# Kernel tuning notes

Measured on AMD Instinct MI355X. Metric: run time of the kernel, lower is better.

The kernel has to match this reference:

```python
import jax, jax.numpy as jnp
import numpy as np

DIM = 1024
NUM_HEADS = 16
HEAD_DIM = DIM // NUM_HEADS  # 64; only used for the softmax scale


def setup_inputs() -> dict:
    key = jax.random.key(0)
    ks = jax.random.split(key, 9)
    s = 1.0 / np.sqrt(DIM)
    return {
        "x": jax.random.normal(ks[0], (2, 4096, DIM), dtype=jnp.float32),
        "Wq": jax.random.normal(ks[1], (DIM, DIM), dtype=jnp.float32) * s,
        "bq": jnp.zeros((DIM,), dtype=jnp.float32),
        "Wk": jax.random.normal(ks[2], (DIM, DIM), dtype=jnp.float32) * s,
        "bk": jnp.zeros((DIM,), dtype=jnp.float32),
        "Wv": jax.random.normal(ks[3], (DIM, DIM), dtype=jnp.float32) * s,
        "bv": jnp.zeros((DIM,), dtype=jnp.float32),
        "Wo": jax.random.normal(ks[4], (DIM, DIM), dtype=jnp.float32) * s,
        "bo": jnp.zeros((DIM,), dtype=jnp.float32),
    }


def reference(x, Wq, bq, Wk, bk, Wv, bv, Wo, bo):
    # Projections (nn.Linear equivalents)
    q = jnp.einsum("bsd,df->bsf", x, Wq) + bq
    k = jnp.einsum("bsd,df->bsf", x, Wk) + bk
    v = jnp.einsum("bsd,df->bsf", x, Wv) + bv
    # Full-dim attention (no head split); scale uses head_dim per original code.
    scale = 1.0 / np.sqrt(HEAD_DIM)
    scores = jnp.einsum("bqd,bkd->bqk", q, k) * scale  # [B, S, S]
    attn = jax.nn.softmax(scores, axis=-1)
    out = jnp.einsum("bqk,bkd->bqd", attn, v)
    return jnp.einsum("bsd,df->bsf", out, Wo) + bo
```

## Files before the change

kernel.cpp:

```cpp
#include <hip/hip_runtime.h>

typedef unsigned short u16;
using bf16x8  = __attribute__((ext_vector_type(8))) __bf16;
using floatx4 = __attribute__((ext_vector_type(4))) float;

__device__ __forceinline__ u16 f2bf(float f) {
  unsigned int u = __builtin_bit_cast(unsigned int, f);
  u += 0x7fffu + ((u >> 16) & 1u);
  return (u16)(u >> 16);
}
__device__ __forceinline__ float bf2f(u16 h) {
  unsigned int u = ((unsigned int)h) << 16;
  return __builtin_bit_cast(float, u);
}

#define AS1(p) ((const __attribute__((address_space(1))) void*)(p))
#define AS3(p) ((__attribute__((address_space(3))) void*)(p))

#define NE2_PROLOGUE(bmv, bnv)                                               \
  __shared__ u16 lds[36864];                          \
  const int tid = threadIdx.x;                                               \
  const int w = tid >> 6, lane = tid & 63;                                   \
  const int wm = (w >> 2) * 64, wn = (w & 3) * 64;                           \
  const int wm4 = (w >> 2) * 4;            \
  const int wn4 = (w & 3) * 4;             \
  const long bm = (bmv), bn = (bnv);                                         \
  floatx4 acc[4][4] = {};                                                    \
  const int fr = lane & 15;                                                  \
  const int kq = (lane >> 4) * 8;                                            \
  const int oc = (lane >> 4) * 4;                                            \
  const int swz  = (lane * 16) ^ (((lane >> 5) & 1) << 5);                   \
  const int srow = swz >> 6;                                                 \
  const int scol = (swz & 63) >> 1;                                          \
  const int st0  = w * 2;                                                    \
  const int aoff = fr * 64 + ((kq * 2) ^ (((fr >> 3) & 1) << 5));

#define NE2_SETUP_PTRS(Abp, Bbp, ldK)                                        \
  const u16* A0p = (Abp) + (long)(w * 16 + srow) * (ldK) + scol;             \
  const u16* B0p = (Bbp) + (long)(st0 * 16 + srow) * (ldK) + scol;           \
  const u16* B1p = B0p + 16L * (ldK);

#define NE2_SA(TT, S)                                                        \
  { u16* d_ = lds + (S) * 12288 + w * 512;                                   \
    __builtin_amdgcn_global_load_lds(AS1(A0p + (long)(TT) * 32), AS3(d_), 16, 0, 0); }
#define NE2_SB(TT, S)                                                        \
  { u16* d_ = lds + (S) * 12288 + 4096 + st0 * 512;                          \
    long o_ = (long)(TT) * 32;                                               \
    __builtin_amdgcn_global_load_lds(AS1(B0p + o_), AS3(d_), 16, 0, 0);      \
    __builtin_amdgcn_global_load_lds(AS1(B1p + o_), AS3(d_ + 512), 16, 0, 0); }

#define NE_MF_SWAP(mi, ni, c) __builtin_amdgcn_mfma_f32_16x16x32_bf16(bf[ni], af[mi], (c), 0, 0, 0)
#define NE_MF_NS(mi, ni, c)   __builtin_amdgcn_mfma_f32_16x16x32_bf16(af[mi], bf[ni], (c), 0, 0, 0)

#define NE2_TILE_G(T, NT, sR, sW, MF)                                        \
  {                                                                          \
    const char* sb_ = (const char*)lds + (sR) * 24576;                       \
    if ((T) + 2 < (NT)) { NE2_SB((T) + 2, sW) NE2_SA((T) + 2, sW) }          \
    bf16x8 af[4], bf[4];                                                     \
    _Pragma("unroll")                                                        \
    for (int i = 0; i < 4; ++i)                                              \
      af[i] = *(const bf16x8*)(sb_ + (wm4 + i) * 1024 + aoff);               \
    _Pragma("unroll")                                                        \
    for (int i = 0; i < 4; ++i)                                              \
      bf[i] = *(const bf16x8*)(sb_ + 8192 + (wn4 + i) * 1024 + aoff);        \
    asm volatile("s_waitcnt lgkmcnt(0)" ::: "memory");                       \
    __builtin_amdgcn_sched_barrier(0);                                       \
    __builtin_amdgcn_s_setprio(1);                                           \
    _Pragma("unroll")                                                        \
    for (int mi = 0; mi < 4; ++mi)                                           \
      _Pragma("unroll")                                                      \
      for (int ni = 0; ni < 4; ++ni)                                         \
        acc[mi][ni] = MF(mi, ni, acc[mi][ni]);                               \
    __builtin_amdgcn_s_setprio(0);                                           \
    if ((T) < (NT) - 2)       { asm volatile("s_waitcnt vmcnt(3)" ::: "memory"); } \
    else if ((T) == (NT) - 2) { asm volatile("s_waitcnt vmcnt(0)" ::: "memory"); } \
    __builtin_amdgcn_s_barrier();                                            \
    __builtin_amdgcn_sched_barrier(0);                                       \
  }

#define NE2_START()                                                          \
  NE2_SA(0, 0) NE2_SB(0, 0) NE2_SA(1, 1) NE2_SB(1, 1)                        \
  asm volatile("s_waitcnt vmcnt(3)" ::: "memory");                           \
  __builtin_amdgcn_s_barrier();                                              \
  __builtin_amdgcn_sched_barrier(0);

#define NE2_LOOP(NT, TILE_MACRO)                                             \
  {                                                                          \
    int sR = 0, sW = 2;                                                      \
    for (int T = 0; T < (NT); ++T) {                                         \
      TILE_MACRO(T, (NT), sR, sW)                                            \
      sR = (sR == 2) ? 0 : sR + 1;                                           \
      sW = (sW == 2) ? 0 : sW + 1;                                           \
    }                                                                        \
  }

#define NE2_TILE(T, NT, sR, sW)    NE2_TILE_G(T, NT, sR, sW, NE_MF_SWAP)
#define NE2_TILE_NS(T, NT, sR, sW) NE2_TILE_G(T, NT, sR, sW, NE_MF_NS)

__global__ __launch_bounds__(512, 4) void gemm_qk_exp(
    const u16* __restrict__ q, const u16* __restrict__ k,
    u16* __restrict__ probs, float* __restrict__ lpartT, float alpha)
{
  const int N = 4096;
  const int xcd = blockIdx.x;
  const int j = blockIdx.y;
  const long b = xcd >> 2;
  const int by = (xcd & 3) * 8 + (j & 7);
  const int bx = j >> 3;

  NE2_PROLOGUE((long)by * 128, (long)bx * 256);
  const u16* Ab = q + b * 4096 * 1024 + bm * 1024;
  const u16* Bb = k + b * 4096 * 1024 + bn * 1024;
  NE2_SETUP_PTRS(Ab, Bb, 1024);
  u16* P = probs + b * 4096L * 4096;
  float* lp = lpartT + b * 4096 * 64;

  NE2_START()
  NE2_LOOP(32, NE2_TILE)

  const float a2 = alpha * 1.44269504f;
  const int cg = bx * 4 + (w & 3);
#pragma unroll
  for (int mi = 0; mi < 4; ++mi) {
    long row = bm + wm + mi * 16 + fr;
    float rs = 0.f;
#pragma unroll
    for (int ni = 0; ni < 4; ++ni) {
      long colb = bn + wn + ni * 16 + oc;
      float e0 = __builtin_amdgcn_exp2f(acc[mi][ni][0] * a2);
      float e1 = __builtin_amdgcn_exp2f(acc[mi][ni][1] * a2);
      float e2 = __builtin_amdgcn_exp2f(acc[mi][ni][2] * a2);
      float e3 = __builtin_amdgcn_exp2f(acc[mi][ni][3] * a2);
      rs += (e0 + e1) + (e2 + e3);
      ushort4 o;
      o.x = f2bf(e0); o.y = f2bf(e1); o.z = f2bf(e2); o.w = f2bf(e3);
      *(ushort4*)(P + row * N + colb) = o;
    }
    rs += __shfl_xor(rs, 16);
    rs += __shfl_xor(rs, 32);
    if (lane < 16)
      lp[(bm + wm + mi * 16 + lane) * 64 + cg] = rs;
  }
}

__global__ __launch_bounds__(512, 4) void gemm_pv_splitk2(
    const u16* __restrict__ probs, const u16* __restrict__ vT,
    u16* __restrict__ pA, u16* __restrict__ pB)
{
  const int xcd = blockIdx.x;
  const int j = blockIdx.y;
  const long b = xcd >> 2;
  const int sp = (xcd >> 1) & 1;
  const int by = (xcd & 1) * 16 + (j & 15);
  const int bx = j >> 4;

  NE2_PROLOGUE((long)by * 128, (long)bx * 256);
  const u16* Ab = probs + b * 4096L * 4096 + bm * 4096 + sp * 2048;
  const u16* Bb = vT + b * 1024L * 4096 + bn * 4096 + sp * 2048;
  NE2_SETUP_PTRS(Ab, Bb, 4096);
  u16* part = (b ? pB : pA) + (long)sp * 4096 * 1024;

  NE2_START()
  NE2_LOOP(64, NE2_TILE)

#pragma unroll
  for (int mi = 0; mi < 4; ++mi) {
    long row = bm + wm + mi * 16 + fr;
#pragma unroll
    for (int ni = 0; ni < 4; ++ni) {
      long colb = bn + wn + ni * 16 + oc;
      ushort4 o;
      o.x = f2bf(acc[mi][ni][0]);
      o.y = f2bf(acc[mi][ni][1]);
      o.z = f2bf(acc[mi][ni][2]);
      o.w = f2bf(acc[mi][ni][3]);
      *(ushort4*)(part + row * 1024 + colb) = o;
    }
  }
}

__global__ __launch_bounds__(512, 4) void gemm_qkv(
    const u16* __restrict__ A, const u16* __restrict__ Bt,
    u16* __restrict__ qb, u16* __restrict__ kb, u16* __restrict__ vT,
    const float* __restrict__ bq, const float* __restrict__ bk,
    const float* __restrict__ bv)
{
  const int xcd = blockIdx.x;
  const int j = blockIdx.y;
  const int by = xcd * 8 + (j & 7);
  const int bx = j >> 3;

  NE2_PROLOGUE((long)by * 128, (long)bx * 256);
  const u16* Ab = A + bm * 1024;
  const u16* Bb = Bt + bn * 1024;
  NE2_SETUP_PTRS(Ab, Bb, 1024);

  if (bn < 2048) {
    NE2_START()
    NE2_LOOP(32, NE2_TILE)
    u16* C = (bn < 1024) ? qb : kb;
    const float* bias = (bn < 1024) ? bq : bk;
#pragma unroll
    for (int mi = 0; mi < 4; ++mi) {
      long row = bm + wm + mi * 16 + fr;
#pragma unroll
      for (int ni = 0; ni < 4; ++ni) {
        long colg = bn + wn + ni * 16 + oc;
        long cc = colg & 1023;
        float4 bv4 = *(const float4*)(bias + cc);
        ushort4 o;
        o.x = f2bf(acc[mi][ni][0] + bv4.x);
        o.y = f2bf(acc[mi][ni][1] + bv4.y);
        o.z = f2bf(acc[mi][ni][2] + bv4.z);
        o.w = f2bf(acc[mi][ni][3] + bv4.w);
        *(ushort4*)(C + row * 1024 + cc) = o;
      }
    }
  } else {
    NE2_START()
    NE2_LOOP(32, NE2_TILE_NS)
    const int orow = (lane >> 4) * 4;
    const long b_ = bm >> 12;
    const long s0 = (bm & 4095) + wm;
    u16* vb = vT + b_ * (1024L * 4096);
#pragma unroll
    for (int ni = 0; ni < 4; ++ni) {
      long d = bn + wn + ni * 16 + fr - 2048;
      float bvv = bv[d];
#pragma unroll
      for (int mi = 0; mi < 4; ++mi) {
        long s = s0 + mi * 16 + orow;
        ushort4 o;
        o.x = f2bf(acc[mi][ni][0] + bvv);
        o.y = f2bf(acc[mi][ni][1] + bvv);
        o.z = f2bf(acc[mi][ni][2] + bvv);
        o.w = f2bf(acc[mi][ni][3] + bvv);
        *(ushort4*)(vb + d * 4096L + s) = o;
      }
    }
  }
}

__global__ __launch_bounds__(512, 4) void gemm_bt(
    const u16* __restrict__ A, const u16* __restrict__ Bt,
    float* __restrict__ Cout, const float* __restrict__ bias)
{
  const int xcd = blockIdx.x;
  const int j = blockIdx.y;
  const int by = xcd * 8 + (j & 7);
  const int bx = j >> 3;

  NE2_PROLOGUE((long)by * 128, (long)bx * 256);
  const u16* Ab = A + bm * 1024;
  const u16* Bb = Bt + bn * 1024;
  NE2_SETUP_PTRS(Ab, Bb, 1024);

  NE2_START()
  NE2_LOOP(32, NE2_TILE)

#pragma unroll
  for (int mi = 0; mi < 4; ++mi) {
    long row = bm + wm + mi * 16 + fr;
#pragma unroll
    for (int ni = 0; ni < 4; ++ni) {
      long colb = bn + wn + ni * 16 + oc;
      float4 bv4 = *(const float4*)(bias + colb);
      float4 o;
      o.x = acc[mi][ni][0] + bv4.x;
      o.y = acc[mi][ni][1] + bv4.y;
      o.z = acc[mi][ni][2] + bv4.z;
      o.w = acc[mi][ni][3] + bv4.w;
      *(float4*)(Cout + row * 1024 + colb) = o;
    }
  }
}

__global__ __launch_bounds__(256) void reduce2_div_row(
    const u16* __restrict__ pA, const u16* __restrict__ pB,
    const float* __restrict__ lpartT, u16* __restrict__ ob)
{
  const int row = blockIdx.x;
  const long b = blockIdx.y;
  const int tid = threadIdx.x;
  const u16* part = b ? pB : pA;
  const float* lp = lpartT + b * 4096 * 64;
  __shared__ float sl;
  if (tid < 64) {
    float s = lp[(long)row * 64 + tid];
#pragma unroll
    for (int off = 32; off; off >>= 1) s += __shfl_down(s, off);
    if (tid == 0) sl = s;
  }
  __syncthreads();
  const float inv = 1.0f / sl;
  const long base = (long)row * 1024 + tid * 4;
  float acc4[4] = {0.f, 0.f, 0.f, 0.f};
#pragma unroll
  for (int s = 0; s < 2; ++s) {
    ushort4 p = *(const ushort4*)(part + (long)s * 4096 * 1024 + base);
    acc4[0] += bf2f(p.x); acc4[1] += bf2f(p.y);
    acc4[2] += bf2f(p.z); acc4[3] += bf2f(p.w);
  }
  ushort4 o;
  o.x = f2bf(acc4[0] * inv);
  o.y = f2bf(acc4[1] * inv);
  o.z = f2bf(acc4[2] * inv);
  o.w = f2bf(acc4[3] * inv);
  *(ushort4*)(ob + b * 4096L * 1024 + base) = o;
}

__global__ __launch_bounds__(256) void prep(
    const float* __restrict__ x, u16* __restrict__ xb,
    const float* __restrict__ W0, const float* __restrict__ W1,
    const float* __restrict__ W2, const float* __restrict__ W3,
    u16* __restrict__ O0, u16* __restrict__ O1,
    u16* __restrict__ O2, u16* __restrict__ O3)
{
  __shared__ float tile[32][33];
  int blk = blockIdx.x;
  if (blk < 8192) {
    int i = blk * 256 + threadIdx.x;
    float4 f = ((const float4*)x)[i];
    ushort4 o;
    o.x = f2bf(f.x); o.y = f2bf(f.y); o.z = f2bf(f.z); o.w = f2bf(f.w);
    ((ushort4*)xb)[i] = o;
  } else {
    blk -= 8192;
    const int z = blk >> 10, t = blk & 1023;
    const float* in = (z == 0) ? W0 : (z == 1) ? W1 : (z == 2) ? W2 : W3;
    u16* outp = (z == 0) ? O0 : (z == 1) ? O1 : (z == 2) ? O2 : O3;
    const int bx = (t & 31) * 32, by = (t >> 5) * 32;
    const int tx = threadIdx.x & 31, ty = threadIdx.x >> 5;
    for (int i = ty; i < 32; i += 8)
      tile[i][tx] = in[(long)(by + i) * 1024 + bx + tx];
    __syncthreads();
    for (int i = ty; i < 32; i += 8)
      outp[(long)(bx + i) * 1024 + by + tx] = f2bf(tile[tx][i]);
  }
}

extern "C" void kernel_launch(void* const* d_in, const int* in_sizes, int n_in,
                              void* d_out, int out_size, void* d_ws, size_t ws_size,
                              hipStream_t stream) {
  const float* x  = (const float*)d_in[0];
  const float* Wq = (const float*)d_in[1];
  const float* bq = (const float*)d_in[2];
  const float* Wk = (const float*)d_in[3];
  const float* bk = (const float*)d_in[4];
  const float* Wv = (const float*)d_in[5];
  const float* bv = (const float*)d_in[6];
  const float* Wo = (const float*)d_in[7];
  const float* bo = (const float*)d_in[8];
  float* out = (float*)d_out;

  const int B = 2, S = 4096, D = 1024;
  const long MB = 1L << 20;

  char* w = (char*)d_ws;
  u16* qb  = (u16*)(w);
  u16* kb  = (u16*)(w + 16 * MB);
  u16* vT  = (u16*)(w + 32 * MB);
  u16* xb  = (u16*)(w + 48 * MB);
  u16* ob  = xb;
  u16* WqkvT = (u16*)(w + 64 * MB);
  u16* WoT = WqkvT + 3072L * 1024;
  u16* probs = (u16*)(w + 72 * MB);
  u16* partA = (u16*)(w);
  u16* partB = (u16*)(w + 136 * MB);
  float* lpartT = (float*)d_out;

  prep<<<dim3(8192 + 4096), 256, 0, stream>>>(
      x, xb, Wq, Wk, Wv, Wo,
      WqkvT, WqkvT + 1024L * 1024, WqkvT + 2048L * 1024, WoT);

  gemm_qkv<<<dim3(8, 96), 512, 0, stream>>>(
      xb, WqkvT, qb, kb, vT, bq, bk, bv);

  const float scale = 0.125f;
  gemm_qk_exp<<<dim3(8, 128), 512, 0, stream>>>(
      qb, kb, probs, lpartT, scale);
  gemm_pv_splitk2<<<dim3(8, 64), 512, 0, stream>>>(
      probs, vT, partA, partB);
  reduce2_div_row<<<dim3(S, B), 256, 0, stream>>>(partA, partB, lpartT, ob);

  gemm_bt<<<dim3(8, 32), 512, 0, stream>>>(ob, WoT, out, bo);
}
```

Before: 363.2 us.

## Enlarge GEMM block tiles to 256x256 with interleaved LDS fragment loads

Moves the QKV, QK-exp and PV GEMMs from 128x256 to 256x256 block tiles. Each wave now computes 128x64, with 8x4 accumulators, and the grids are halved to match. Inside the tile loop, A-fragment LDS reads are interleaved with MFMA groups in a rotating three-register scheme so LDS latency hides behind matrix math instead of a full lgkmcnt(0) wait. This raises arithmetic intensity per LDS and global byte, but needs more registers and 96KB of LDS, so occupancy drops (launch bounds 4 to 2). With fewer blocks the wave count per CU may leave the GPU underfilled.

```diff
diff --git a/kernel.cpp b/kernel.cpp
--- a/kernel.cpp
+++ b/kernel.cpp
@@ -16,14 +16,109 @@
 
 #define AS1(p) ((const __attribute__((address_space(1))) void*)(p))
 #define AS3(p) ((__attribute__((address_space(3))) void*)(p))
+#define SGB()  __builtin_amdgcn_sched_barrier(0)
+
+#define NE3_PROLOGUE(bmv, bnv)                                               \
+  __shared__ u16 lds[49152];                    \
+  const int tid = threadIdx.x;                                               \
+  const int w = tid >> 6, lane = tid & 63;                                   \
+  const int wm = (w >> 2) * 128, wn = (w & 3) * 64;                          \
+  const int wm16 = (w >> 2) * 8;           \
+  const int wn4  = (w & 3) * 4;            \
+  const long bm = (bmv), bn = (bnv);                                         \
+  floatx4 acc[8][4] = {};                                                    \
+  const int fr = lane & 15;                                                  \
+  const int kq = (lane >> 4) * 8;                                            \
+  const int oc = (lane >> 4) * 4;                                            \
+  const int swz  = (lane * 16) ^ (((lane >> 5) & 1) << 5);                   \
+  const int srow = swz >> 6;                                                 \
+  const int scol = (swz & 63) >> 1;                                          \
+  const int st0  = w * 2;                                                    \
+  const int aoff = fr * 64 + ((kq * 2) ^ (((fr >> 3) & 1) << 5));
+
+#define NE3_SETUP_PTRS(Abp, Bbp, ldK)                                        \
+  const u16* A0p = (Abp) + (long)(st0 * 16 + srow) * (ldK) + scol;           \
+  const u16* A1p = A0p + 16L * (ldK);                                        \
+  const u16* B0p = (Bbp) + (long)(st0 * 16 + srow) * (ldK) + scol;           \
+  const u16* B1p = B0p + 16L * (ldK);
+
+#define NE3_SA(TT, S)                                                        \
+  { u16* d_ = lds + (S) * 16384 + st0 * 512;                                 \
+    long o_ = (long)(TT) * 32;                                               \
+    __builtin_amdgcn_global_load_lds(AS1(A0p + o_), AS3(d_), 16, 0, 0);      \
+    __builtin_amdgcn_global_load_lds(AS1(A1p + o_), AS3(d_ + 512), 16, 0, 0); }
+#define NE3_SB(TT, S)                                                        \
+  { u16* d_ = lds + (S) * 16384 + 8192 + st0 * 512;                          \
+    long o_ = (long)(TT) * 32;                                               \
+    __builtin_amdgcn_global_load_lds(AS1(B0p + o_), AS3(d_), 16, 0, 0);      \
+    __builtin_amdgcn_global_load_lds(AS1(B1p + o_), AS3(d_ + 512), 16, 0, 0); }
+
+#define MFOP_SWAP(b_, a_, c_) __builtin_amdgcn_mfma_f32_16x16x32_bf16((b_), (a_), (c_), 0, 0, 0)
+#define MFOP_NS(b_, a_, c_)   __builtin_amdgcn_mfma_f32_16x16x32_bf16((a_), (b_), (c_), 0, 0, 0)
+
+#define NE3_MM(kk, AREG, MFOP)                                               \
+    acc[kk][0] = MFOP(bf[0], AREG, acc[kk][0]);                              \
+    acc[kk][1] = MFOP(bf[1], AREG, acc[kk][1]);                              \
+    acc[kk][2] = MFOP(bf[2], AREG, acc[kk][2]);                              \
+    acc[kk][3] = MFOP(bf[3], AREG, acc[kk][3]);
+
+#define NE3_TILE_G(T, NT, sR, sW, MFOP)                                      \
+  {                                                                          \
+    const char* sb_ = (const char*)lds + (sR) * 32768;                       \
+    if ((T) + 2 < (NT)) { NE3_SB((T) + 2, sW) NE3_SA((T) + 2, sW) }          \
+    bf16x8 bf[4], afA, afB, afC;                                             \
+    bf[0] = *(const bf16x8*)(sb_ + 16384 + (wn4 + 0) * 1024 + aoff);         \
+    bf[1] = *(const bf16x8*)(sb_ + 16384 + (wn4 + 1) * 1024 + aoff);         \
+    bf[2] = *(const bf16x8*)(sb_ + 16384 + (wn4 + 2) * 1024 + aoff);         \
+    bf[3] = *(const bf16x8*)(sb_ + 16384 + (wn4 + 3) * 1024 + aoff);         \
+    afA = *(const bf16x8*)(sb_ + (wm16 + 0) * 1024 + aoff);                  \
+    afB = *(const bf16x8*)(sb_ + (wm16 + 1) * 1024 + aoff);                  \
+    SGB();                                                                   \
+    __builtin_amdgcn_s_setprio(1);                                           \
+    afC = *(const bf16x8*)(sb_ + (wm16 + 2) * 1024 + aoff);                  \
+    SGB(); NE3_MM(0, afA, MFOP) SGB();                                       \
+    afA = *(const bf16x8*)(sb_ + (wm16 + 3) * 1024 + aoff);                  \
+    SGB(); NE3_MM(1, afB, MFOP) SGB();                                       \
+    afB = *(const bf16x8*)(sb_ + (wm16 + 4) * 1024 + aoff);                  \
+    SGB(); NE3_MM(2, afC, MFOP) SGB();                                       \
+    afC = *(const bf16x8*)(sb_ + (wm16 + 5) * 1024 + aoff);                  \
+    SGB(); NE3_MM(3, afA, MFOP) SGB();                                       \
+    afA = *(const bf16x8*)(sb_ + (wm16 + 6) * 1024 + aoff);                  \
+    SGB(); NE3_MM(4, afB, MFOP) SGB();                                       \
+    afB = *(const bf16x8*)(sb_ + (wm16 + 7) * 1024 + aoff);                  \
+    SGB(); NE3_MM(5, afC, MFOP) SGB();                                       \
+    NE3_MM(6, afA, MFOP) SGB();                                              \
+    NE3_MM(7, afB, MFOP)                                                     \
+    __builtin_amdgcn_s_setprio(0);                                           \
+    if ((T) < (NT) - 2)       { asm volatile("s_waitcnt vmcnt(4)" ::: "memory"); } \
+    else if ((T) == (NT) - 2) { asm volatile("s_waitcnt vmcnt(0)" ::: "memory"); } \
+    __builtin_amdgcn_s_barrier();                                            \
+    SGB();                                                                   \
+  }
+
+#define NE3_START()                                                          \
+  NE3_SA(0, 0) NE3_SB(0, 0) NE3_SA(1, 1) NE3_SB(1, 1)                        \
+  asm volatile("s_waitcnt vmcnt(4)" ::: "memory");                           \
+  __builtin_amdgcn_s_barrier();                                              \
+  SGB();
+
+#define NE3_LOOP(NT, MFOP)                                                   \
+  {                                                                          \
+    int sR = 0, sW = 2;                                                      \
+    for (int T = 0; T < (NT); ++T) {                                         \
+      NE3_TILE_G(T, (NT), sR, sW, MFOP)                                      \
+      sR = (sR == 2) ? 0 : sR + 1;                                           \
+      sW = (sW == 2) ? 0 : sW + 1;                                           \
+    }                                                                        \
+  }
 
 #define NE2_PROLOGUE(bmv, bnv)                                               \
   __shared__ u16 lds[36864];                          \
   const int tid = threadIdx.x;                                               \
   const int w = tid >> 6, lane = tid & 63;                                   \
   const int wm = (w >> 2) * 64, wn = (w & 3) * 64;                           \
-  const int wm4 = (w >> 2) * 4;            \
-  const int wn4 = (w & 3) * 4;             \
+  const int wm4 = (w >> 2) * 4;                                              \
+  const int wn4 = (w & 3) * 4;                                               \
   const long bm = (bmv), bn = (bnv);                                         \
   floatx4 acc[4][4] = {};                                                    \
   const int fr = lane & 15;                                                  \
@@ -50,7 +145,6 @@
     __builtin_amdgcn_global_load_lds(AS1(B1p + o_), AS3(d_ + 512), 16, 0, 0); }
 
 #define NE_MF_SWAP(mi, ni, c) __builtin_amdgcn_mfma_f32_16x16x32_bf16(bf[ni], af[mi], (c), 0, 0, 0)
-#define NE_MF_NS(mi, ni, c)   __builtin_amdgcn_mfma_f32_16x16x32_bf16(af[mi], bf[ni], (c), 0, 0, 0)
 
 #define NE2_TILE_G(T, NT, sR, sW, MF)                                        \
   {                                                                          \
@@ -64,7 +158,7 @@
     for (int i = 0; i < 4; ++i)                                              \
       bf[i] = *(const bf16x8*)(sb_ + 8192 + (wn4 + i) * 1024 + aoff);        \
     asm volatile("s_waitcnt lgkmcnt(0)" ::: "memory");                       \
-    __builtin_amdgcn_sched_barrier(0);                                       \
+    SGB();                                                                   \
     __builtin_amdgcn_s_setprio(1);                                           \
     _Pragma("unroll")                                                        \
     for (int mi = 0; mi < 4; ++mi)                                           \
@@ -75,14 +169,14 @@
     if ((T) < (NT) - 2)       { asm volatile("s_waitcnt vmcnt(3)" ::: "memory"); } \
     else if ((T) == (NT) - 2) { asm volatile("s_waitcnt vmcnt(0)" ::: "memory"); } \
     __builtin_amdgcn_s_barrier();                                            \
-    __builtin_amdgcn_sched_barrier(0);                                       \
+    SGB();                                                                   \
   }
 
 #define NE2_START()                                                          \
   NE2_SA(0, 0) NE2_SB(0, 0) NE2_SA(1, 1) NE2_SB(1, 1)                        \
   asm volatile("s_waitcnt vmcnt(3)" ::: "memory");                           \
   __builtin_amdgcn_s_barrier();                                              \
-  __builtin_amdgcn_sched_barrier(0);
+  SGB();
 
 #define NE2_LOOP(NT, TILE_MACRO)                                             \
   {                                                                          \
@@ -94,10 +188,9 @@
     }                                                                        \
   }
 
-#define NE2_TILE(T, NT, sR, sW)    NE2_TILE_G(T, NT, sR, sW, NE_MF_SWAP)
-#define NE2_TILE_NS(T, NT, sR, sW) NE2_TILE_G(T, NT, sR, sW, NE_MF_NS)
-
-__global__ __launch_bounds__(512, 4) void gemm_qk_exp(
+#define NE2_TILE(T, NT, sR, sW) NE2_TILE_G(T, NT, sR, sW, NE_MF_SWAP)
+
+__global__ __launch_bounds__(512, 2) void gemm_qk_exp(
     const u16* __restrict__ q, const u16* __restrict__ k,
     u16* __restrict__ probs, float* __restrict__ lpartT, float alpha)
 {
@@ -105,23 +198,23 @@
   const int xcd = blockIdx.x;
   const int j = blockIdx.y;
   const long b = xcd >> 2;
-  const int by = (xcd & 3) * 8 + (j & 7);
-  const int bx = j >> 3;
-
-  NE2_PROLOGUE((long)by * 128, (long)bx * 256);
+  const int by = (xcd & 3) * 4 + (j & 3);
+  const int bx = j >> 2;
+
+  NE3_PROLOGUE((long)by * 256, (long)bx * 256);
   const u16* Ab = q + b * 4096 * 1024 + bm * 1024;
   const u16* Bb = k + b * 4096 * 1024 + bn * 1024;
-  NE2_SETUP_PTRS(Ab, Bb, 1024);
+  NE3_SETUP_PTRS(Ab, Bb, 1024);
   u16* P = probs + b * 4096L * 4096;
   float* lp = lpartT + b * 4096 * 64;
 
-  NE2_START()
-  NE2_LOOP(32, NE2_TILE)
+  NE3_START()
+  NE3_LOOP(32, MFOP_SWAP)
 
   const float a2 = alpha * 1.44269504f;
   const int cg = bx * 4 + (w & 3);
 #pragma unroll
-  for (int mi = 0; mi < 4; ++mi) {
+  for (int mi = 0; mi < 8; ++mi) {
     long row = bm + wm + mi * 16 + fr;
     float rs = 0.f;
 #pragma unroll
@@ -143,7 +236,7 @@
   }
 }
 
-__global__ __launch_bounds__(512, 4) void gemm_pv_splitk2(
+__global__ __launch_bounds__(512, 2) void gemm_pv_splitk2(
     const u16* __restrict__ probs, const u16* __restrict__ vT,
     u16* __restrict__ pA, u16* __restrict__ pB)
 {
@@ -151,20 +244,20 @@
   const int j = blockIdx.y;
   const long b = xcd >> 2;
   const int sp = (xcd >> 1) & 1;
-  const int by = (xcd & 1) * 16 + (j & 15);
-  const int bx = j >> 4;
-
-  NE2_PROLOGUE((long)by * 128, (long)bx * 256);
+  const int by = (xcd & 1) * 8 + (j & 7);
+  const int bx = j >> 3;
+
+  NE3_PROLOGUE((long)by * 256, (long)bx * 256);
   const u16* Ab = probs + b * 4096L * 4096 + bm * 4096 + sp * 2048;
   const u16* Bb = vT + b * 1024L * 4096 + bn * 4096 + sp * 2048;
-  NE2_SETUP_PTRS(Ab, Bb, 4096);
+  NE3_SETUP_PTRS(Ab, Bb, 4096);
   u16* part = (b ? pB : pA) + (long)sp * 4096 * 1024;
 
-  NE2_START()
-  NE2_LOOP(64, NE2_TILE)
-
-#pragma unroll
-  for (int mi = 0; mi < 4; ++mi) {
+  NE3_START()
+  NE3_LOOP(64, MFOP_SWAP)
+
+#pragma unroll
+  for (int mi = 0; mi < 8; ++mi) {
     long row = bm + wm + mi * 16 + fr;
 #pragma unroll
     for (int ni = 0; ni < 4; ++ni) {
@@ -179,7 +272,7 @@
   }
 }
 
-__global__ __launch_bounds__(512, 4) void gemm_qkv(
+__global__ __launch_bounds__(512, 2) void gemm_qkv(
     const u16* __restrict__ A, const u16* __restrict__ Bt,
     u16* __restrict__ qb, u16* __restrict__ kb, u16* __restrict__ vT,
     const float* __restrict__ bq, const float* __restrict__ bk,
@@ -187,21 +280,21 @@
 {
   const int xcd = blockIdx.x;
   const int j = blockIdx.y;
-  const int by = xcd * 8 + (j & 7);
-  const int bx = j >> 3;
-
-  NE2_PROLOGUE((long)by * 128, (long)bx * 256);
+  const int by = xcd * 4 + (j & 3);
+  const int bx = j >> 2;
+
+  NE3_PROLOGUE((long)by * 256, (long)bx * 256);
   const u16* Ab = A + bm * 1024;
   const u16* Bb = Bt + bn * 1024;
-  NE2_SETUP_PTRS(Ab, Bb, 1024);
+  NE3_SETUP_PTRS(Ab, Bb, 1024);
 
   if (bn < 2048) {
-    NE2_START()
-    NE2_LOOP(32, NE2_TILE)
+    NE3_START()
+    NE3_LOOP(32, MFOP_SWAP)
     u16* C = (bn < 1024) ? qb : kb;
     const float* bias = (bn < 1024) ? bq : bk;
 #pragma unroll
-    for (int mi = 0; mi < 4; ++mi) {
+    for (int mi = 0; mi < 8; ++mi) {
       long row = bm + wm + mi * 16 + fr;
 #pragma unroll
       for (int ni = 0; ni < 4; ++ni) {
@@ -217,8 +310,8 @@
       }
     }
   } else {
-    NE2_START()
-    NE2_LOOP(32, NE2_TILE_NS)
+    NE3_START()
+    NE3_LOOP(32, MFOP_NS)
     const int orow = (lane >> 4) * 4;
     const long b_ = bm >> 12;
     const long s0 = (bm & 4095) + wm;
@@ -228,7 +321,7 @@
       long d = bn + wn + ni * 16 + fr - 2048;
       float bvv = bv[d];
 #pragma unroll
-      for (int mi = 0; mi < 4; ++mi) {
+      for (int mi = 0; mi < 8; ++mi) {
         long s = s0 + mi * 16 + orow;
         ushort4 o;
         o.x = f2bf(acc[mi][ni][0] + bvv);
@@ -373,13 +466,13 @@
       x, xb, Wq, Wk, Wv, Wo,
       WqkvT, WqkvT + 1024L * 1024, WqkvT + 2048L * 1024, WoT);
 
-  gemm_qkv<<<dim3(8, 96), 512, 0, stream>>>(
+  gemm_qkv<<<dim3(8, 48), 512, 0, stream>>>(
       xb, WqkvT, qb, kb, vT, bq, bk, bv);
 
   const float scale = 0.125f;
-  gemm_qk_exp<<<dim3(8, 128), 512, 0, stream>>>(
+  gemm_qk_exp<<<dim3(8, 64), 512, 0, stream>>>(
       qb, kb, probs, lpartT, scale);
-  gemm_pv_splitk2<<<dim3(8, 64), 512, 0, stream>>>(
+  gemm_pv_splitk2<<<dim3(8, 32), 512, 0, stream>>>(
       probs, vT, partA, partB);
   reduce2_div_row<<<dim3(S, B), 256, 0, stream>>>(partA, partB, lpartT, ob);
 
```

Result: faster. 352.3 us (-3.0%).
